# Kernel tuning notes

Hardware: AMD Instinct MI355X
Metric: run time of the kernel (lower is better)

## Reference

```python
import jax, jax.numpy as jnp
import numpy as np
from jax import lax

D = 512      # inter_dim
E = 768      # expand_dim
S = 256      # squeeze_dim
BUCKET = 64
N_BLOCK = 6

def layernorm(x, g, b, eps):
    m = jnp.mean(x, axis=-1, keepdims=True)
    v = jnp.mean(jnp.square(x - m), axis=-1, keepdims=True)
    return (x - m) / jnp.sqrt(v + eps) * g + b

def setup_inputs():
    key = jax.random.key(0)
    ks = jax.random.split(key, 12)
    B, N, IN = 4, 4096, 768
    def rn(k, shape, scale):
        return jax.random.normal(k, shape, dtype=jnp.float32) * scale
    return {
        "xs": jax.random.normal(ks[0], (B, N, IN), dtype=jnp.float32),
        # in1: Linear(IN, D) + LayerNorm(eps=1e-8) + LeakyReLU(0.1)
        "W_in": rn(ks[1], (IN, D), IN ** -0.5), "b_in": jnp.zeros(D),
        "ln_in_g": jnp.ones(D), "ln_in_b": jnp.zeros(D),
        # 6 GAU (FlashQuadAttention) blocks, params stacked on leading axis
        "blk_ln_g": jnp.ones((N_BLOCK, D)), "blk_ln_b": jnp.zeros((N_BLOCK, D)),
        "blk_Wuv": rn(ks[2], (N_BLOCK, D, 2 * E + S), D ** -0.5),
        "blk_buv": jnp.zeros((N_BLOCK, 2 * E + S)),
        "blk_gamma": jnp.ones((N_BLOCK, 2, S)) + rn(ks[3], (N_BLOCK, 2, S), 0.02),
        "blk_beta": rn(ks[4], (N_BLOCK, 2, S), 0.02),
        "blk_Wo": rn(ks[5], (N_BLOCK, E, D), E ** -0.5),
        "blk_bo": jnp.zeros((N_BLOCK, D)),
        # tr_layer (applied inside tree loop)
        "tr_W": rn(ks[6], (D, D), D ** -0.5), "tr_b": jnp.zeros(D),
        "tr_a": jnp.full((), 1e-6, dtype=jnp.float32),
        # out1 = TransLayer + Linear(D, out_dim)
        "tr2_W": rn(ks[7], (D, D), D ** -0.5), "tr2_b": jnp.zeros(D),
        "tr2_a": jnp.full((), 1e-6, dtype=jnp.float32),
        "out_W": rn(ks[8], (D, 2), D ** -0.5), "out_b": jnp.zeros(2),
    }

def reference(xs, W_in, b_in, ln_in_g, ln_in_b,
              blk_ln_g, blk_ln_b, blk_Wuv, blk_buv, blk_gamma, blk_beta,
              blk_Wo, blk_bo, tr_W, tr_b, tr_a, tr2_W, tr2_b, tr2_a,
              out_W, out_b):
    def subnet(h):  # h: [n_buckets, BUCKET, D]
        def step(h, p):
            lg, lb, Wuv, buv, gam, bet, Wo, bo = p
            n = layernorm(h, lg, lb, 1e-5)
            uvb = jax.nn.silu(n @ Wuv + buv)
            u, v, base = uvb[..., :E], uvb[..., E:2 * E], uvb[..., 2 * E:]
            q = base * gam[0] + bet[0]
            k = base * gam[1] + bet[1]
            Lq = h.shape[1]
            a = jnp.square(jax.nn.relu(jnp.einsum('gls,gms->glm', q, k) / Lq))
            o = jnp.einsum('glm,gme->gle', a, v) * u
            return h + o @ Wo + bo, None
        h, _ = lax.scan(step, h, (blk_ln_g, blk_ln_b, blk_Wuv, blk_buv,
                                  blk_gamma, blk_beta, blk_Wo, blk_bo))
        return h

    def tr_layer(x, W, b, a):
        return x + jax.nn.gelu(x @ W + b, approximate=False) * a

    def run_sample(x):  # x: [N, in_dim]
        h = layernorm(x @ W_in + b_in, ln_in_g, ln_in_b, 1e-8)
        h = jnp.where(h > 0, h, 0.1 * h)  # LeakyReLU(0.1)
        seq = h
        ys = []
        while seq.shape[0] > 1:  # static shapes -> unrolled tree levels
            ids = jnp.argsort(jnp.linalg.norm(seq, axis=-1))  # sort by L2 norm
            buckets = seq[ids].reshape(-1, BUCKET, D)
            gy = subnet(buckets).mean(axis=1)           # [n_buckets, D]
            ys.append(tr_layer(gy, tr_W, tr_b, tr_a).mean(axis=0))
            seq = gy
        return jnp.stack(ys, 0).mean(0)  # [D]

    y = jax.vmap(run_sample)(xs)          # [B, D]
    y = tr_layer(y, tr2_W, tr2_b, tr2_a)  # out1 TransLayer
    return y @ out_W + out_b              # [B, out_dim]
```

## Files before the change

kernel.cpp:

```cpp
#include <hip/hip_runtime.h>
#include <math.h>

#define R1C 16384

enum { OP_STORE = 0, OP_SILU = 1, OP_RESID = 2, OP_TR = 3 };

typedef _Float16 f16x8 __attribute__((ext_vector_type(8)));
typedef float f32x4 __attribute__((ext_vector_type(4)));

__device__ __forceinline__ float silu_f(float x) { return x / (1.0f + __expf(-x)); }
__device__ __forceinline__ float gelu_f(float x) {
  return 0.5f * x * (1.0f + erff(x * 0.70710678118654752f));
}

__device__ __forceinline__ void gll16(const void* g, const void* l) {
  __builtin_amdgcn_global_load_lds(
      (const __attribute__((address_space(1))) unsigned int*)g,
      (__attribute__((address_space(3))) unsigned int*)l, 16, 0, 0);
}

__device__ __forceinline__ void xcd_swizzle(int& bx, int& by) {
  int nx = gridDim.x;
  int nwg = nx * gridDim.y;
  int flat = by * nx + bx;
  int q = nwg >> 3, r = nwg & 7;
  int xcd = flat & 7, pos = flat >> 3;
  int lbid = (xcd < r) ? xcd * (q + 1) + pos
                       : r * (q + 1) + (xcd - r) * q + pos;
  bx = lbid % nx;
  by = lbid / nx;
}


__global__ __launch_bounds__(256) void gemm_f16(
    const _Float16* __restrict__ A, int lda,
    const _Float16* __restrict__ Bt, int ldb,
    float* __restrict__ C, int ldc, int K,
    const float* __restrict__ bias, int mode,
    const int* __restrict__ ids)
{
  const int BUF = 128 * 32;
  __shared__ _Float16 As[2 * BUF];
  __shared__ _Float16 Bs[2 * BUF];
  int bx = blockIdx.x, by = blockIdx.y;
  xcd_swizzle(bx, by);
  int tid = threadIdx.x;
  int lane = tid & 63, w = tid >> 6;
  int wm = w >> 1, wn = w & 1;
  int row0 = by * 128, col0 = bx * 128;

  int sm0 = tid >> 2;
  int sk  = (((tid & 3) - (sm0 >> 1)) & 3) * 8;
  const _Float16* gA[2];
  const _Float16* gB[2];
  gA[0] = A + (size_t)(row0 + sm0) * lda + sk;
  gA[1] = A + (size_t)(row0 + 64 + sm0) * lda + sk;
  gB[0] = Bt + (size_t)(col0 + sm0) * ldb + sk;
  gB[1] = Bt + (size_t)(col0 + 64 + sm0) * ldb + sk;
  const _Float16* lA[2] = { As + (size_t)(w * 64) * 8, As + (size_t)(256 + w * 64) * 8 };
  const _Float16* lB[2] = { Bs + (size_t)(w * 64) * 8, Bs + (size_t)(256 + w * 64) * 8 };

  int mrow = lane & 15, quad = lane >> 4;
  const f16x8* aptr[4];
  const f16x8* bptr[4];
#pragma unroll
  for (int t = 0; t < 4; ++t) {
    int ml = wm * 64 + t * 16 + mrow;
    aptr[t] = (const f16x8*)(As + (size_t)(ml * 4 + ((quad + (ml >> 1)) & 3)) * 8);
    int nl = wn * 64 + t * 16 + mrow;
    bptr[t] = (const f16x8*)(Bs + (size_t)(nl * 4 + ((quad + (nl >> 1)) & 3)) * 8);
  }

  f32x4 acc[4][4] = {};

  gll16(gA[0], lA[0]); gll16(gA[1], lA[1]);
  gll16(gB[0], lB[0]); gll16(gB[1], lB[1]);
  gA[0] += 32; gA[1] += 32; gB[0] += 32; gB[1] += 32;

  for (int kt = 0; kt < K; kt += 32) {
    int cur = (kt >> 5) & 1;
    __syncthreads();
    if (kt + 32 < K) {
      int nxo = (cur ^ 1) * BUF;
      gll16(gA[0], lA[0] + nxo); gll16(gA[1], lA[1] + nxo);
      gll16(gB[0], lB[0] + nxo); gll16(gB[1], lB[1] + nxo);
      gA[0] += 32; gA[1] += 32; gB[0] += 32; gB[1] += 32;
    }
    int fo = cur * (BUF / 8);
    f16x8 af[4], bfr[4];
#pragma unroll
    for (int t = 0; t < 4; ++t) { af[t] = *(aptr[t] + fo); bfr[t] = *(bptr[t] + fo); }
#pragma unroll
    for (int mt = 0; mt < 4; ++mt)
#pragma unroll
      for (int nt = 0; nt < 4; ++nt)
        acc[mt][nt] = __builtin_amdgcn_mfma_f32_16x16x32_f16(
            af[mt], bfr[nt], acc[mt][nt], 0, 0, 0);
  }

#pragma unroll
  for (int mt = 0; mt < 4; ++mt) {
#pragma unroll
    for (int nt = 0; nt < 4; ++nt) {
      int c = col0 + wn * 64 + nt * 16 + mrow;
      float bv = bias ? bias[c] : 0.0f;
#pragma unroll
      for (int reg = 0; reg < 4; ++reg) {
        int r = row0 + wm * 64 + mt * 16 + quad * 4 + reg;
        float val = acc[mt][nt][reg] + bv;
        if (mode == OP_STORE) {
          C[(size_t)r * ldc + c] = val;
        } else if (mode == OP_SILU) {
          C[(size_t)r * ldc + c] = silu_f(val);
        } else {
          int hr = ids ? ids[r] : r;
          C[(size_t)hr * ldc + c] += val;
        }
      }
    }
  }
}

__global__ __launch_bounds__(512) void gemm_f16_split(
    const _Float16* __restrict__ Ah, const _Float16* __restrict__ Al, int lda,
    const _Float16* __restrict__ Bh, const _Float16* __restrict__ Bl, int ldb,
    float* __restrict__ C, int ldc, int K, const float* __restrict__ bias)
{
  const int BUF = 128 * 32;
  __shared__ _Float16 AsH[2 * BUF], AsL[2 * BUF];
  __shared__ _Float16 BsH[2 * BUF], BsL[2 * BUF];
  int bx = blockIdx.x, by = blockIdx.y;
  xcd_swizzle(bx, by);
  int tid = threadIdx.x;
  int lane = tid & 63, w = tid >> 6;
  int wm = w >> 1, wn = w & 1;
  int row0 = by * 128, col0 = bx * 128;

  int m0 = tid >> 2;
  int k0e = (((tid & 3) - (m0 >> 1)) & 3) * 8;
  size_t a0 = (size_t)(row0 + m0) * lda + k0e;
  size_t b0 = (size_t)(col0 + m0) * ldb + k0e;
  size_t l0 = (size_t)(w * 64) * 8;

  int mrow = lane & 15, quad = lane >> 4;
  size_t aoff[2], boff[4];
#pragma unroll
  for (int t = 0; t < 2; ++t) {
    int ml = wm * 32 + t * 16 + mrow;
    aoff[t] = (size_t)(ml * 4 + ((quad + (ml >> 1)) & 3)) * 8;
  }
#pragma unroll
  for (int nt = 0; nt < 4; ++nt) {
    int nl = wn * 64 + nt * 16 + mrow;
    boff[nt] = (size_t)(nl * 4 + ((quad + (nl >> 1)) & 3)) * 8;
  }

  f32x4 acc[2][4] = {};

  gll16(Ah + a0, AsH + l0); gll16(Al + a0, AsL + l0);
  gll16(Bh + b0, BsH + l0); gll16(Bl + b0, BsL + l0);
  a0 += 32; b0 += 32;

  for (int kt = 0; kt < K; kt += 32) {
    int cur = (kt >> 5) & 1;
    __syncthreads();
    if (kt + 32 < K) {
      size_t o = (size_t)(cur ^ 1) * BUF;
      gll16(Ah + a0, AsH + l0 + o); gll16(Al + a0, AsL + l0 + o);
      gll16(Bh + b0, BsH + l0 + o); gll16(Bl + b0, BsL + l0 + o);
      a0 += 32; b0 += 32;
    }
    size_t o = (size_t)cur * BUF;
    f16x8 ah[2], al_[2], bh[4], bl[4];
#pragma unroll
    for (int t = 0; t < 2; ++t) {
      ah[t]  = *(const f16x8*)(AsH + aoff[t] + o);
      al_[t] = *(const f16x8*)(AsL + aoff[t] + o);
    }
#pragma unroll
    for (int nt = 0; nt < 4; ++nt) {
      bh[nt] = *(const f16x8*)(BsH + boff[nt] + o);
      bl[nt] = *(const f16x8*)(BsL + boff[nt] + o);
    }
#pragma unroll
    for (int mt = 0; mt < 2; ++mt)
#pragma unroll
      for (int nt = 0; nt < 4; ++nt) {
        acc[mt][nt] = __builtin_amdgcn_mfma_f32_16x16x32_f16(
            ah[mt], bh[nt], acc[mt][nt], 0, 0, 0);
        acc[mt][nt] = __builtin_amdgcn_mfma_f32_16x16x32_f16(
            ah[mt], bl[nt], acc[mt][nt], 0, 0, 0);
        acc[mt][nt] = __builtin_amdgcn_mfma_f32_16x16x32_f16(
            al_[mt], bh[nt], acc[mt][nt], 0, 0, 0);
      }
  }

#pragma unroll
  for (int mt = 0; mt < 2; ++mt)
#pragma unroll
    for (int nt = 0; nt < 4; ++nt) {
      int c = col0 + wn * 64 + nt * 16 + mrow;
      float bv = bias ? bias[c] : 0.0f;
#pragma unroll
      for (int reg = 0; reg < 4; ++reg) {
        int r = row0 + wm * 32 + mt * 16 + quad * 4 + reg;
        C[(size_t)r * ldc + c] = acc[mt][nt][reg] + bv;
      }
    }
}

__global__ __launch_bounds__(256) void gemm_f16_uvb(
    const _Float16* __restrict__ A, int lda,
    const _Float16* __restrict__ Bt,
    int c0, int nu,
    _Float16* __restrict__ ub, _Float16* __restrict__ vb, float* __restrict__ baseb,
    int CH, int K, const float* __restrict__ buv)
{
  const int BUF = 128 * 32;
  __shared__ _Float16 As[2 * BUF];
  __shared__ _Float16 Bs[2 * BUF];
  int bx = blockIdx.x, by = blockIdx.y;
  xcd_swizzle(bx, by);
  int tid = threadIdx.x;
  int lane = tid & 63, w = tid >> 6;
  int wm = w >> 1, wn = w & 1;
  int row0 = by * 128;

  int x = bx;
  int xl, regbase, ldc_, is_base = 0;
  _Float16* dst16 = nullptr;
  if (x < nu)            { xl = x;          regbase = c0;        dst16 = ub; ldc_ = CH; }
  else if (x < 2 * nu)   { xl = x - nu;     regbase = 768 + c0;  dst16 = vb; ldc_ = CH; }
  else                   { xl = x - 2 * nu; regbase = 1536;      is_base = 1; ldc_ = 256; }
  int brow0 = regbase + xl * 128;
  int dcol0 = xl * 128;

  int sm0 = tid >> 2;
  int sk  = (((tid & 3) - (sm0 >> 1)) & 3) * 8;
  const _Float16* gA[2];
  const _Float16* gB[2];
  gA[0] = A + (size_t)(row0 + sm0) * lda + sk;
  gA[1] = A + (size_t)(row0 + 64 + sm0) * lda + sk;
  gB[0] = Bt + (size_t)(brow0 + sm0) * 512 + sk;
  gB[1] = Bt + (size_t)(brow0 + 64 + sm0) * 512 + sk;
  const _Float16* lA[2] = { As + (size_t)(w * 64) * 8, As + (size_t)(256 + w * 64) * 8 };
  const _Float16* lB[2] = { Bs + (size_t)(w * 64) * 8, Bs + (size_t)(256 + w * 64) * 8 };

  int mrow = lane & 15, quad = lane >> 4;
  const f16x8* aptr[4];
  const f16x8* bptr[4];
#pragma unroll
  for (int t = 0; t < 4; ++t) {
    int ml = wm * 64 + t * 16 + mrow;
    aptr[t] = (const f16x8*)(As + (size_t)(ml * 4 + ((quad + (ml >> 1)) & 3)) * 8);
    int nl = wn * 64 + t * 16 + mrow;
    bptr[t] = (const f16x8*)(Bs + (size_t)(nl * 4 + ((quad + (nl >> 1)) & 3)) * 8);
  }

  f32x4 acc[4][4] = {};

  gll16(gA[0], lA[0]); gll16(gA[1], lA[1]);
  gll16(gB[0], lB[0]); gll16(gB[1], lB[1]);
  gA[0] += 32; gA[1] += 32; gB[0] += 32; gB[1] += 32;

  for (int kt = 0; kt < K; kt += 32) {
    int cur = (kt >> 5) & 1;
    __syncthreads();
    if (kt + 32 < K) {
      int nxo = (cur ^ 1) * BUF;
      gll16(gA[0], lA[0] + nxo); gll16(gA[1], lA[1] + nxo);
      gll16(gB[0], lB[0] + nxo); gll16(gB[1], lB[1] + nxo);
      gA[0] += 32; gA[1] += 32; gB[0] += 32; gB[1] += 32;
    }
    int fo = cur * (BUF / 8);
    f16x8 af[4], bfr[4];
#pragma unroll
    for (int t = 0; t < 4; ++t) { af[t] = *(aptr[t] + fo); bfr[t] = *(bptr[t] + fo); }
#pragma unroll
    for (int mt = 0; mt < 4; ++mt)
#pragma unroll
      for (int nt = 0; nt < 4; ++nt)
        acc[mt][nt] = __builtin_amdgcn_mfma_f32_16x16x32_f16(
            af[mt], bfr[nt], acc[mt][nt], 0, 0, 0);
  }

#pragma unroll
  for (int mt = 0; mt < 4; ++mt) {
#pragma unroll
    for (int nt = 0; nt < 4; ++nt) {
      int lc = wn * 64 + nt * 16 + mrow;
      float bv = buv[brow0 + lc];
#pragma unroll
      for (int reg = 0; reg < 4; ++reg) {
        int r = row0 + wm * 64 + mt * 16 + quad * 4 + reg;
        float val = silu_f(acc[mt][nt][reg] + bv);
        if (is_base) baseb[(size_t)r * 256 + dcol0 + lc] = val;
        else         dst16[(size_t)r * ldc_ + dcol0 + lc] = (_Float16)val;
      }
    }
  }
}

__global__ __launch_bounds__(256) void attnapply_fused(
    const float* __restrict__ base, const float* __restrict__ gb,
    const float* __restrict__ bb, const _Float16* __restrict__ v,
    const _Float16* __restrict__ u, _Float16* __restrict__ t, int CH, int ech)
{
  __shared__ _Float16 smem[3 * 64 * 72];
  _Float16* qs = smem;
  _Float16* ks = smem + 64 * 72;
  _Float16* al = smem + 2 * 64 * 72;
  _Float16* vT = smem;

  int bx = blockIdx.x, by = blockIdx.y;
  xcd_swizzle(bx, by);
  int g = by, tid = threadIdx.x;
  int e_lo = bx * ech, e_hi = e_lo + ech;
  int lane = tid & 63, w = tid >> 6;
  int mrow = lane & 15, quad = lane >> 4;
  int srow = tid >> 2, scol = (tid & 3) * 16;

  f32x4 acc[4] = {};
  for (int s0 = 0; s0 < 256; s0 += 64) {
    const float* bp = base + ((size_t)g * 64 + srow) * 256 + s0 + scol;
#pragma unroll
    for (int j4 = 0; j4 < 4; ++j4) {
      float4 xv = *(const float4*)(bp + j4 * 4);
      float xx[4] = {xv.x, xv.y, xv.z, xv.w};
#pragma unroll
      for (int j = 0; j < 4; ++j) {
        int s = s0 + scol + j4 * 4 + j;
        qs[srow * 72 + scol + j4 * 4 + j] = (_Float16)(xx[j] * gb[s] + bb[s]);
        ks[srow * 72 + scol + j4 * 4 + j] = (_Float16)(xx[j] * gb[256 + s] + bb[256 + s]);
      }
    }
    __syncthreads();
#pragma unroll
    for (int ks2 = 0; ks2 < 2; ++ks2) {
      f16x8 aq = *(const f16x8*)(qs + (w * 16 + mrow) * 72 + ks2 * 32 + quad * 8);
#pragma unroll
      for (int nt = 0; nt < 4; ++nt) {
        f16x8 bk = *(const f16x8*)(ks + (nt * 16 + mrow) * 72 + ks2 * 32 + quad * 8);
        acc[nt] = __builtin_amdgcn_mfma_f32_16x16x32_f16(aq, bk, acc[nt], 0, 0, 0);
      }
    }
    __syncthreads();
  }
#pragma unroll
  for (int nt = 0; nt < 4; ++nt)
#pragma unroll
    for (int reg = 0; reg < 4; ++reg) {
      float val = acc[nt][reg] * (1.0f / 64.0f);
      val = val > 0.0f ? val : 0.0f;
      val = val * val;
      al[(w * 16 + quad * 4 + reg) * 72 + nt * 16 + mrow] = (_Float16)val;
    }
  __syncthreads();

  for (int e0 = e_lo; e0 < e_hi; e0 += 64) {
    const _Float16* vp = v + ((size_t)g * 64 + srow) * CH + e0 + scol;
    f16x8 x0 = *(const f16x8*)vp;
    f16x8 x1 = *(const f16x8*)(vp + 8);
#pragma unroll
    for (int j = 0; j < 8; ++j) {
      vT[(scol + j) * 72 + srow] = x0[j];
      vT[(scol + 8 + j) * 72 + srow] = x1[j];
    }
    __syncthreads();
    f32x4 acc2[4] = {};
#pragma unroll
    for (int ks2 = 0; ks2 < 2; ++ks2) {
      f16x8 af = *(const f16x8*)(al + (w * 16 + mrow) * 72 + ks2 * 32 + quad * 8);
#pragma unroll
      for (int nt = 0; nt < 4; ++nt) {
        f16x8 bf = *(const f16x8*)(vT + (nt * 16 + mrow) * 72 + ks2 * 32 + quad * 8);
        acc2[nt] = __builtin_amdgcn_mfma_f32_16x16x32_f16(af, bf, acc2[nt], 0, 0, 0);
      }
    }
#pragma unroll
    for (int nt = 0; nt < 4; ++nt)
#pragma unroll
      for (int reg = 0; reg < 4; ++reg) {
        int row = w * 16 + quad * 4 + reg;
        int col = e0 + nt * 16 + mrow;
        size_t idx = ((size_t)g * 64 + row) * CH + col;
        t[idx] = (_Float16)(acc2[nt][reg] * (float)u[idx]);
      }
    __syncthreads();
  }
}

__global__ __launch_bounds__(256) void gemm_f32(
    const float* __restrict__ A, int lda,
    const float* __restrict__ B, int ldb,
    float* __restrict__ C, int ldc,
    int M, int N, int K,
    const float* __restrict__ bias, int mode,
    const int* __restrict__ ids,
    const float* __restrict__ X,
    const float* __restrict__ alpha)
{
  __shared__ float As[16][68];
  __shared__ float Bs[16][68];
  int tid = threadIdx.x;
  int tx = tid & 15, ty = tid >> 4;
  int col0 = blockIdx.x * 64, row0 = blockIdx.y * 64;
  float acc[4][4] = {};
  int arow = tid >> 2;
  int ak   = (tid & 3) * 4;
  int bk   = tid >> 4;
  int bn   = (tid & 15) * 4;

  for (int kt = 0; kt < K; kt += 16) {
    float4 av = make_float4(0.f, 0.f, 0.f, 0.f);
    if (row0 + arow < M)
      av = *(const float4*)&A[(size_t)(row0 + arow) * lda + kt + ak];
    As[ak + 0][arow] = av.x; As[ak + 1][arow] = av.y;
    As[ak + 2][arow] = av.z; As[ak + 3][arow] = av.w;
    float4 bv = *(const float4*)&B[(size_t)(kt + bk) * ldb + col0 + bn];
    *(float4*)&Bs[bk][bn] = bv;
    __syncthreads();
#pragma unroll
    for (int k = 0; k < 16; ++k) {
      const float4 a4 = *(const float4*)&As[k][ty * 4];
      const float4 b4 = *(const float4*)&Bs[k][tx * 4];
      float a_[4] = {a4.x, a4.y, a4.z, a4.w};
      float b_[4] = {b4.x, b4.y, b4.z, b4.w};
#pragma unroll
      for (int i = 0; i < 4; ++i)
#pragma unroll
        for (int j = 0; j < 4; ++j)
          acc[i][j] = fmaf(a_[i], b_[j], acc[i][j]);
    }
    __syncthreads();
  }

#pragma unroll
  for (int i = 0; i < 4; ++i) {
    int r = row0 + ty * 4 + i;
    if (r >= M) continue;
#pragma unroll
    for (int j = 0; j < 4; ++j) {
      int c = col0 + tx * 4 + j;
      float val = acc[i][j] + (bias ? bias[c] : 0.0f);
      if (mode == OP_STORE) {
        C[(size_t)r * ldc + c] = val;
      } else if (mode == OP_SILU) {
        C[(size_t)r * ldc + c] = silu_f(val);
      } else if (mode == OP_RESID) {
        int hr = ids ? ids[r] : r;
        C[(size_t)hr * ldc + c] += val;
      } else {
        C[(size_t)r * ldc + c] = X[(size_t)r * ldc + c] + gelu_f(val) * alpha[0];
      }
    }
  }
}

__global__ __launch_bounds__(256) void transpose_cast(
    const float* __restrict__ in, _Float16* __restrict__ out, int K, int N)
{
  in  += (size_t)blockIdx.z * K * N;
  out += (size_t)blockIdx.z * K * N;
  __shared__ float t[32][33];
  int k0 = blockIdx.y * 32, n0 = blockIdx.x * 32;
  int tx = threadIdx.x & 31, ty = threadIdx.x >> 5;
  for (int i = ty; i < 32; i += 8) {
    int k = k0 + i, n = n0 + tx;
    t[i][tx] = (k < K && n < N) ? in[(size_t)k * N + n] : 0.0f;
  }
  __syncthreads();
  for (int i = ty; i < 32; i += 8) {
    int n = n0 + i, k = k0 + tx;
    if (n < N && k < K) out[(size_t)n * K + k] = (_Float16)t[tx][i];
  }
}

__global__ __launch_bounds__(256) void transpose_split(
    const float* __restrict__ in, _Float16* __restrict__ hi,
    _Float16* __restrict__ lo, int K, int N)
{
  __shared__ float t[32][33];
  int k0 = blockIdx.y * 32, n0 = blockIdx.x * 32;
  int tx = threadIdx.x & 31, ty = threadIdx.x >> 5;
  for (int i = ty; i < 32; i += 8) {
    int k = k0 + i, n = n0 + tx;
    t[i][tx] = (k < K && n < N) ? in[(size_t)k * N + n] : 0.0f;
  }
  __syncthreads();
  for (int i = ty; i < 32; i += 8) {
    int n = n0 + i, k = k0 + tx;
    if (n < N && k < K) {
      float x = t[tx][i];
      _Float16 h = (_Float16)x;
      hi[(size_t)n * K + k] = h;
      lo[(size_t)n * K + k] = (_Float16)(x - (float)h);
    }
  }
}

__global__ __launch_bounds__(256) void split_f16_kernel(
    const float* __restrict__ in, _Float16* __restrict__ hi,
    _Float16* __restrict__ lo, int n)
{
  int i = blockIdx.x * 256 + threadIdx.x;
  if (i < n) {
    float x = in[i];
    _Float16 h = (_Float16)x;
    hi[i] = h;
    lo[i] = (_Float16)(x - (float)h);
  }
}

template <typename OUT>
__global__ __launch_bounds__(256) void ln_kernel(
    const float* __restrict__ src, const int* __restrict__ ids,
    OUT* __restrict__ dst, const float* __restrict__ g,
    const float* __restrict__ b, float eps, int leaky,
    float* __restrict__ nrm2)
{
  int r = blockIdx.x;
  int sr = ids ? ids[r] : r;
  int tid = threadIdx.x;
  float v0 = src[(size_t)sr * 512 + tid];
  float v1 = src[(size_t)sr * 512 + tid + 256];
  __shared__ float red[256], red2[256];
  red[tid] = v0 + v1;
  red2[tid] = v0 * v0 + v1 * v1;
  __syncthreads();
  for (int s = 128; s > 0; s >>= 1) {
    if (tid < s) { red[tid] += red[tid + s]; red2[tid] += red2[tid + s]; }
    __syncthreads();
  }
  float mean = red[0] * (1.0f / 512.0f);
  float var  = red2[0] * (1.0f / 512.0f) - mean * mean;
  float rs = rsqrtf(var + eps);
  float o0 = (v0 - mean) * rs * g[tid] + b[tid];
  float o1 = (v1 - mean) * rs * g[tid + 256] + b[tid + 256];
  if (leaky) {
    o0 = o0 > 0.0f ? o0 : 0.1f * o0;
    o1 = o1 > 0.0f ? o1 : 0.1f * o1;
  }
  dst[(size_t)r * 512 + tid] = (OUT)o0;
  dst[(size_t)r * 512 + tid + 256] = (OUT)o1;
  if (nrm2) {
    __syncthreads();
    red[tid] = o0 * o0 + o1 * o1;
    __syncthreads();
    for (int s = 128; s > 0; s >>= 1) {
      if (tid < s) red[tid] += red[tid + s];
      __syncthreads();
    }
    if (tid == 0) nrm2[r] = red[0];
  }
}

__global__ __launch_bounds__(128) void permute_rows(
    const float* __restrict__ src, const int* __restrict__ ids,
    float* __restrict__ dst)
{
  int r = blockIdx.x, sr = ids[r];
  const float4* s = (const float4*)(src + (size_t)sr * 512);
  float4* d = (float4*)(dst + (size_t)r * 512);
  d[threadIdx.x] = s[threadIdx.x];
}

__global__ __launch_bounds__(1024) void sort_kernel(const float* __restrict__ norm2,
                                                    int* __restrict__ ids)
{
  __shared__ float key[4096];
  __shared__ int   val[4096];
  int s = blockIdx.x, tid = threadIdx.x;
  for (int i = tid; i < 4096; i += 1024) { key[i] = norm2[s * 4096 + i]; val[i] = i; }
  __syncthreads();
  for (int len = 2; len <= 4096; len <<= 1) {
    for (int j = len >> 1; j > 0; j >>= 1) {
      for (int t = tid; t < 2048; t += 1024) {
        int i1 = (t << 1) - (t & (j - 1));
        int i2 = i1 + j;
        bool up = ((i1 & len) == 0);
        float ka = key[i1], kb = key[i2];
        int va = val[i1], vb = val[i2];
        bool gt = (ka > kb) || (ka == kb && va > vb);
        if (gt == up) {
          key[i1] = kb; key[i2] = ka;
          val[i1] = vb; val[i2] = va;
        }
      }
      __syncthreads();
    }
  }
  for (int i = tid; i < 4096; i += 1024) ids[s * 4096 + i] = s * 4096 + val[i];
}

__global__ __launch_bounds__(256) void bucketmean_kernel(
    const float* __restrict__ src, const int* __restrict__ ids,
    float* __restrict__ dst)
{
  int g = blockIdx.x, tid = threadIdx.x;
  float s0 = 0.0f, s1 = 0.0f;
  for (int i = 0; i < 64; ++i) {
    int r = g * 64 + i;
    if (ids) r = ids[r];
    s0 += src[(size_t)r * 512 + tid];
    s1 += src[(size_t)r * 512 + tid + 256];
  }
  dst[(size_t)g * 512 + tid] = s0 * (1.0f / 64.0f);
  dst[(size_t)g * 512 + tid + 256] = s1 * (1.0f / 64.0f);
}

__global__ void avg_kernel(const float* __restrict__ a, const float* __restrict__ b,
                           float* __restrict__ o, int n)
{
  int i = blockIdx.x * 256 + threadIdx.x;
  if (i < n) o[i] = 0.5f * (a[i] + b[i]);
}

__global__ void out_kernel(const float* __restrict__ y, const float* __restrict__ W,
                           const float* __restrict__ b, float* __restrict__ out)
{
  int tid = threadIdx.x;
  if (tid < 8) {
    int s = tid >> 1, j = tid & 1;
    float acc = b[j];
    for (int d = 0; d < 512; ++d) acc += y[s * 512 + d] * W[d * 2 + j];
    out[s * 2 + j] = acc;
  }
}

extern "C" void kernel_launch(void* const* d_in, const int* in_sizes, int n_in,
                              void* d_out, int out_size, void* d_ws, size_t ws_size,
                              hipStream_t stream)
{
  const float* xs       = (const float*)d_in[0];
  const float* W_in     = (const float*)d_in[1];
  const float* b_in     = (const float*)d_in[2];
  const float* ln_in_g  = (const float*)d_in[3];
  const float* ln_in_b  = (const float*)d_in[4];
  const float* blk_ln_g = (const float*)d_in[5];
  const float* blk_ln_b = (const float*)d_in[6];
  const float* blk_Wuv  = (const float*)d_in[7];
  const float* blk_buv  = (const float*)d_in[8];
  const float* blk_gam  = (const float*)d_in[9];
  const float* blk_bet  = (const float*)d_in[10];
  const float* blk_Wo   = (const float*)d_in[11];
  const float* blk_bo   = (const float*)d_in[12];
  const float* tr_W     = (const float*)d_in[13];
  const float* tr_b     = (const float*)d_in[14];
  const float* tr_a     = (const float*)d_in[15];
  const float* tr2_W    = (const float*)d_in[16];
  const float* tr2_b    = (const float*)d_in[17];
  const float* tr2_a    = (const float*)d_in[18];
  const float* out_W    = (const float*)d_in[19];
  const float* out_b    = (const float*)d_in[20];
  float* outp = (float*)d_out;

  const size_t R1 = R1C;

  char* wsb = (char*)d_ws;
  size_t off = 0;
  auto carve = [&](size_t bytes) {
    char* r = wsb + off;
    off = (off + bytes + 255) & ~(size_t)255;
    return (void*)r;
  };
  float* h      = (float*)carve(R1 * 512 * 4);
  float* hslot  = (float*)carve(R1 * 512 * 4);
  float* norm2b = (float*)carve(R1 * 4);
  int*   idsb   = (int*)carve(R1 * 4);
  float* gy     = (float*)carve((size_t)256 * 512 * 4);
  float* tl     = (float*)carve((size_t)256 * 512 * 4);
  float* gy2    = (float*)carve(4 * 512 * 4);
  float* ys0    = (float*)carve(4 * 512 * 4);
  float* ys1    = (float*)carve(4 * 512 * 4);
  float* yv     = (float*)carve(4 * 512 * 4);
  float* y2     = (float*)carve(4 * 512 * 4);
  _Float16* Wuvt = (_Float16*)carve((size_t)6 * 1792 * 512 * 2);
  _Float16* Wot  = (_Float16*)carve((size_t)6 * 512 * 768 * 2);
  size_t persistent = off;

  size_t stageA_sorted = 2 * R1 * 768 * 2 + 2 * (size_t)512 * 768 * 2 + R1 * 512 * 4 + 2048;
  size_t block768 = R1 * 256 * 4 + 3 * R1 * (size_t)768 * 2 + 2048;
  size_t un_sorted = stageA_sorted > block768 ? stageA_sorted : block768;
  bool sorted_mode = (persistent + un_sorted + 4096 <= ws_size);

  int CH = 768;
  bool splitA = true;
  if (!sorted_mode) {
    size_t stageA_fb = 2 * R1 * 768 * 2 + 2 * (size_t)512 * 768 * 2 + 1024;
    auto block_bytes = [&](size_t ch) {
      return R1 * 256 * 4 + 3 * R1 * ch * 2 + 2048;
    };
    CH = 0; splitA = false;
    const int cand[4] = {768, 384, 256, 128};
    for (int ci = 0; ci < 4; ++ci) {
      size_t bb2 = block_bytes(cand[ci]);
      size_t un2 = bb2 > stageA_fb ? bb2 : stageA_fb;
      if (persistent + un2 + 4096 <= ws_size) { CH = cand[ci]; splitA = true; break; }
    }
    if (!CH) {
      for (int ci = 0; ci < 4; ++ci)
        if (persistent + block_bytes(cand[ci]) + 4096 <= ws_size) { CH = cand[ci]; break; }
      if (!CH) CH = 128;
    }
  }
  int nu = CH / 128;
  int ech = CH >= 256 ? 256 : CH;
  int nch = CH / ech;

  char* un = wsb + ((persistent + 255) & ~(size_t)255);
  _Float16* xs_hi = (_Float16*)un;
  _Float16* xs_lo = xs_hi + R1 * 768;
  _Float16* Wt_hi = xs_lo + R1 * 768;
  _Float16* Wt_lo = Wt_hi + (size_t)512 * 768;
  float*    nbA   = sorted_mode ? (float*)(Wt_lo + (size_t)512 * 768) : hslot;
  float*    baseb = (float*)un;
  _Float16* ub    = (_Float16*)(un + R1 * 256 * 4);
  _Float16* vb    = ub + R1 * (size_t)CH;
  _Float16* tb    = vb + R1 * (size_t)CH;
  _Float16* nbuf  = sorted_mode ? tb : (_Float16*)hslot;
  float* hres = sorted_mode ? hslot : h;
  const int* blkids = sorted_mode ? nullptr : idsb;

  dim3 blk(256);
  dim3 blk5(512);

  transpose_cast<<<dim3(56, 16, 6), blk, 0, stream>>>(blk_Wuv, Wuvt, 512, 1792);
  transpose_cast<<<dim3(16, 24, 6), blk, 0, stream>>>(blk_Wo, Wot, 768, 512);

  if (splitA) {
    split_f16_kernel<<<(int)(R1 * 768 / 256), blk, 0, stream>>>(xs, xs_hi, xs_lo,
                                                                (int)(R1 * 768));
    transpose_split<<<dim3(16, 24, 1), blk, 0, stream>>>(W_in, Wt_hi, Wt_lo, 768, 512);
    gemm_f16_split<<<dim3(4, 128), blk5, 0, stream>>>(xs_hi, xs_lo, 768,
        Wt_hi, Wt_lo, 768, nbA, 512, 768, b_in);
  } else {
    gemm_f32<<<dim3(8, 256), blk, 0, stream>>>(xs, 768, W_in, 512, nbA, 512,
        16384, 512, 768, b_in, OP_STORE, nullptr, nullptr, nullptr);
  }
  ln_kernel<float><<<16384, 256, 0, stream>>>(nbA, nullptr, h, ln_in_g, ln_in_b,
                                              1e-8f, 1, norm2b);
  sort_kernel<<<4, 1024, 0, stream>>>(norm2b, idsb);
  if (sorted_mode)
    permute_rows<<<16384, 128, 0, stream>>>(h, idsb, hres);

  for (int b = 0; b < 6; ++b) {
    const _Float16* Wuv_t = Wuvt + (size_t)b * 1792 * 512;
    const float*    buv   = blk_buv + b * 1792;
    const _Float16* Wo_t  = Wot + (size_t)b * 512 * 768;
    ln_kernel<_Float16><<<16384, 256, 0, stream>>>(hres, blkids, nbuf,
        blk_ln_g + b * 512, blk_ln_b + b * 512, 1e-5f, 0, nullptr);
    for (int c0 = 0; c0 < 768; c0 += CH) {
      int incl = (c0 == 0) ? 2 : 0;
      gemm_f16_uvb<<<dim3(2 * nu + incl, 128), blk, 0, stream>>>(nbuf, 512, Wuv_t,
          c0, nu, ub, vb, baseb, CH, 512, buv);
      attnapply_fused<<<dim3(nch, 256), blk, 0, stream>>>(baseb, blk_gam + b * 512,
          blk_bet + b * 512, vb, ub, tb, CH, ech);
      const float* bo = (c0 + CH == 768) ? (blk_bo + b * 512) : nullptr;
      gemm_f16<<<dim3(4, 128), blk, 0, stream>>>(tb, CH, Wo_t + c0, 768,
          hres, 512, CH, bo, OP_RESID, blkids);
    }
  }
  bucketmean_kernel<<<256, 256, 0, stream>>>(hres, blkids, gy);

  gemm_f32<<<dim3(8, 4), blk, 0, stream>>>(gy, 512, tr_W, 512, tl, 512,
      256, 512, 512, tr_b, OP_TR, nullptr, gy, tr_a);
  bucketmean_kernel<<<4, 256, 0, stream>>>(tl, nullptr, ys0);

  for (int b = 0; b < 6; ++b) {
    const _Float16* Wuv_t = Wuvt + (size_t)b * 1792 * 512;
    const float*    buv   = blk_buv + b * 1792;
    const _Float16* Wo_t  = Wot + (size_t)b * 512 * 768;
    ln_kernel<_Float16><<<256, 256, 0, stream>>>(gy, nullptr, nbuf, blk_ln_g + b * 512,
                                                 blk_ln_b + b * 512, 1e-5f, 0, nullptr);
    for (int c0 = 0; c0 < 768; c0 += CH) {
      int incl = (c0 == 0) ? 2 : 0;
      gemm_f16_uvb<<<dim3(2 * nu + incl, 2), blk, 0, stream>>>(nbuf, 512, Wuv_t,
          c0, nu, ub, vb, baseb, CH, 512, buv);
      attnapply_fused<<<dim3(nch, 4), blk, 0, stream>>>(baseb, blk_gam + b * 512,
          blk_bet + b * 512, vb, ub, tb, CH, ech);
      const float* bo = (c0 + CH == 768) ? (blk_bo + b * 512) : nullptr;
      gemm_f16<<<dim3(4, 2), blk, 0, stream>>>(tb, CH, Wo_t + c0, 768,
          gy, 512, CH, bo, OP_RESID, nullptr);
    }
  }
  bucketmean_kernel<<<4, 256, 0, stream>>>(gy, nullptr, gy2);

  gemm_f32<<<dim3(8, 1), blk, 0, stream>>>(gy2, 512, tr_W, 512, ys1, 512,
      4, 512, 512, tr_b, OP_TR, nullptr, gy2, tr_a);
  avg_kernel<<<8, 256, 0, stream>>>(ys0, ys1, yv, 2048);
  gemm_f32<<<dim3(8, 1), blk, 0, stream>>>(yv, 512, tr2_W, 512, y2, 512,
      4, 512, 512, tr2_b, OP_TR, nullptr, yv, tr2_a);
  out_kernel<<<1, 64, 0, stream>>>(y2, out_W, out_b, outp);
}
```

Measured before the change: 1.747 ms.

## Triple-buffer LDS in f16 GEMM kernels with explicit vmcnt waits

Replaces the double-buffered global-to-LDS K loop in gemm_f16 and gemm_f16_uvb with a three-stage ring buffer that keeps two tiles in flight. It uses explicit s_waitcnt vmcnt(4) and a raw s_barrier instead of __syncthreads. Launch bounds now request 3 blocks per SIMD. The aim is to hide global load latency behind the MFMA work. In exchange, LDS use rises to 48KB per block, which may limit occupancy, and the hand-written waitcnt logic depends on the exact count of outstanding loads.

After: 1.757 ms. Within noise of the previous version (+0.5%).

```diff
diff --git a/kernel.cpp b/kernel.cpp
--- a/kernel.cpp
+++ b/kernel.cpp
@@ -32,7 +32,38 @@
 }
 
 
-__global__ __launch_bounds__(256) void gemm_f16(
+#define STAGE4(slot) do {                                            \
+    gll16(gAa, lAa + (slot) * BUF); gll16(gAb, lAb + (slot) * BUF);  \
+    gll16(gBa, lBa + (slot) * BUF); gll16(gBb, lBb + (slot) * BUF);  \
+    gAa += 32; gAb += 32; gBa += 32; gBb += 32; } while (0)
+
+#define KLOOP4()                                                          \
+  int ntile = K >> 5;                                                     \
+  STAGE4(0);                                                              \
+  if (ntile > 1) STAGE4(1);                                               \
+  int cur = 0;                                                            \
+  for (int t = 0; t < ntile; ++t) {                                       \
+    if (t + 1 < ntile) asm volatile("s_waitcnt vmcnt(4)" ::: "memory");   \
+    else               asm volatile("s_waitcnt vmcnt(0)" ::: "memory");   \
+    __builtin_amdgcn_s_barrier();                                         \
+    __builtin_amdgcn_sched_barrier(0);                                    \
+    if (t + 2 < ntile) { int pf = cur + 2; if (pf >= 3) pf -= 3; STAGE4(pf); } \
+    int fo = cur * (BUF / 8);                                             \
+    f16x8 af[4], bfr[4];                                                  \
+    _Pragma("unroll")                                                     \
+    for (int tt = 0; tt < 4; ++tt) af[tt] = *(aptr[tt] + fo);             \
+    _Pragma("unroll")                                                     \
+    for (int tt = 0; tt < 4; ++tt) bfr[tt] = *(bptr[tt] + fo);            \
+    _Pragma("unroll")                                                     \
+    for (int mt = 0; mt < 4; ++mt)                                        \
+      _Pragma("unroll")                                                   \
+      for (int nt = 0; nt < 4; ++nt)                                      \
+        acc[mt][nt] = __builtin_amdgcn_mfma_f32_16x16x32_f16(             \
+            af[mt], bfr[nt], acc[mt][nt], 0, 0, 0);                       \
+    cur = (cur == 2) ? 0 : cur + 1;                                       \
+  }
+
+__global__ __launch_bounds__(256, 3) void gemm_f16(
     const _Float16* __restrict__ A, int lda,
     const _Float16* __restrict__ Bt, int ldb,
     float* __restrict__ C, int ldc, int K,
@@ -40,8 +71,8 @@
     const int* __restrict__ ids)
 {
   const int BUF = 128 * 32;
-  __shared__ _Float16 As[2 * BUF];
-  __shared__ _Float16 Bs[2 * BUF];
+  __shared__ _Float16 As[3 * BUF];
+  __shared__ _Float16 Bs[3 * BUF];
   int bx = blockIdx.x, by = blockIdx.y;
   xcd_swizzle(bx, by);
   int tid = threadIdx.x;
@@ -49,16 +80,16 @@
   int wm = w >> 1, wn = w & 1;
   int row0 = by * 128, col0 = bx * 128;
 
-  int sm0 = tid >> 2;
-  int sk  = (((tid & 3) - (sm0 >> 1)) & 3) * 8;
-  const _Float16* gA[2];
-  const _Float16* gB[2];
-  gA[0] = A + (size_t)(row0 + sm0) * lda + sk;
-  gA[1] = A + (size_t)(row0 + 64 + sm0) * lda + sk;
-  gB[0] = Bt + (size_t)(col0 + sm0) * ldb + sk;
-  gB[1] = Bt + (size_t)(col0 + 64 + sm0) * ldb + sk;
-  const _Float16* lA[2] = { As + (size_t)(w * 64) * 8, As + (size_t)(256 + w * 64) * 8 };
-  const _Float16* lB[2] = { Bs + (size_t)(w * 64) * 8, Bs + (size_t)(256 + w * 64) * 8 };
+  int m0 = tid >> 2;
+  int k0e = (((tid & 3) - (m0 >> 1)) & 3) * 8;
+  const _Float16* gAa = A + (size_t)(row0 + m0) * lda + k0e;
+  const _Float16* gAb = A + (size_t)(row0 + 64 + m0) * lda + k0e;
+  const _Float16* gBa = Bt + (size_t)(col0 + m0) * ldb + k0e;
+  const _Float16* gBb = Bt + (size_t)(col0 + 64 + m0) * ldb + k0e;
+  const _Float16* lAa = As + (size_t)(w * 64) * 8;
+  const _Float16* lAb = As + (size_t)(256 + w * 64) * 8;
+  const _Float16* lBa = Bs + (size_t)(w * 64) * 8;
+  const _Float16* lBb = Bs + (size_t)(256 + w * 64) * 8;
 
   int mrow = lane & 15, quad = lane >> 4;
   const f16x8* aptr[4];
@@ -73,30 +104,7 @@
 
   f32x4 acc[4][4] = {};
 
-  gll16(gA[0], lA[0]); gll16(gA[1], lA[1]);
-  gll16(gB[0], lB[0]); gll16(gB[1], lB[1]);
-  gA[0] += 32; gA[1] += 32; gB[0] += 32; gB[1] += 32;
-
-  for (int kt = 0; kt < K; kt += 32) {
-    int cur = (kt >> 5) & 1;
-    __syncthreads();
-    if (kt + 32 < K) {
-      int nxo = (cur ^ 1) * BUF;
-      gll16(gA[0], lA[0] + nxo); gll16(gA[1], lA[1] + nxo);
-      gll16(gB[0], lB[0] + nxo); gll16(gB[1], lB[1] + nxo);
-      gA[0] += 32; gA[1] += 32; gB[0] += 32; gB[1] += 32;
-    }
-    int fo = cur * (BUF / 8);
-    f16x8 af[4], bfr[4];
-#pragma unroll
-    for (int t = 0; t < 4; ++t) { af[t] = *(aptr[t] + fo); bfr[t] = *(bptr[t] + fo); }
-#pragma unroll
-    for (int mt = 0; mt < 4; ++mt)
-#pragma unroll
-      for (int nt = 0; nt < 4; ++nt)
-        acc[mt][nt] = __builtin_amdgcn_mfma_f32_16x16x32_f16(
-            af[mt], bfr[nt], acc[mt][nt], 0, 0, 0);
-  }
+  KLOOP4();
 
 #pragma unroll
   for (int mt = 0; mt < 4; ++mt) {
@@ -209,7 +217,7 @@
     }
 }
 
-__global__ __launch_bounds__(256) void gemm_f16_uvb(
+__global__ __launch_bounds__(256, 3) void gemm_f16_uvb(
     const _Float16* __restrict__ A, int lda,
     const _Float16* __restrict__ Bt,
     int c0, int nu,
@@ -217,8 +225,8 @@
     int CH, int K, const float* __restrict__ buv)
 {
   const int BUF = 128 * 32;
-  __shared__ _Float16 As[2 * BUF];
-  __shared__ _Float16 Bs[2 * BUF];
+  __shared__ _Float16 As[3 * BUF];
+  __shared__ _Float16 Bs[3 * BUF];
   int bx = blockIdx.x, by = blockIdx.y;
   xcd_swizzle(bx, by);
   int tid = threadIdx.x;
@@ -235,16 +243,16 @@
   int brow0 = regbase + xl * 128;
   int dcol0 = xl * 128;
 
-  int sm0 = tid >> 2;
-  int sk  = (((tid & 3) - (sm0 >> 1)) & 3) * 8;
-  const _Float16* gA[2];
-  const _Float16* gB[2];
-  gA[0] = A + (size_t)(row0 + sm0) * lda + sk;
-  gA[1] = A + (size_t)(row0 + 64 + sm0) * lda + sk;
-  gB[0] = Bt + (size_t)(brow0 + sm0) * 512 + sk;
-  gB[1] = Bt + (size_t)(brow0 + 64 + sm0) * 512 + sk;
-  const _Float16* lA[2] = { As + (size_t)(w * 64) * 8, As + (size_t)(256 + w * 64) * 8 };
-  const _Float16* lB[2] = { Bs + (size_t)(w * 64) * 8, Bs + (size_t)(256 + w * 64) * 8 };
+  int m0 = tid >> 2;
+  int k0e = (((tid & 3) - (m0 >> 1)) & 3) * 8;
+  const _Float16* gAa = A + (size_t)(row0 + m0) * lda + k0e;
+  const _Float16* gAb = A + (size_t)(row0 + 64 + m0) * lda + k0e;
+  const _Float16* gBa = Bt + (size_t)(brow0 + m0) * 512 + k0e;
+  const _Float16* gBb = Bt + (size_t)(brow0 + 64 + m0) * 512 + k0e;
+  const _Float16* lAa = As + (size_t)(w * 64) * 8;
+  const _Float16* lAb = As + (size_t)(256 + w * 64) * 8;
+  const _Float16* lBa = Bs + (size_t)(w * 64) * 8;
+  const _Float16* lBb = Bs + (size_t)(256 + w * 64) * 8;
 
   int mrow = lane & 15, quad = lane >> 4;
   const f16x8* aptr[4];
@@ -259,30 +267,7 @@
 
   f32x4 acc[4][4] = {};
 
-  gll16(gA[0], lA[0]); gll16(gA[1], lA[1]);
-  gll16(gB[0], lB[0]); gll16(gB[1], lB[1]);
-  gA[0] += 32; gA[1] += 32; gB[0] += 32; gB[1] += 32;
-
-  for (int kt = 0; kt < K; kt += 32) {
-    int cur = (kt >> 5) & 1;
-    __syncthreads();
-    if (kt + 32 < K) {
-      int nxo = (cur ^ 1) * BUF;
-      gll16(gA[0], lA[0] + nxo); gll16(gA[1], lA[1] + nxo);
-      gll16(gB[0], lB[0] + nxo); gll16(gB[1], lB[1] + nxo);
-      gA[0] += 32; gA[1] += 32; gB[0] += 32; gB[1] += 32;
-    }
-    int fo = cur * (BUF / 8);
-    f16x8 af[4], bfr[4];
-#pragma unroll
-    for (int t = 0; t < 4; ++t) { af[t] = *(aptr[t] + fo); bfr[t] = *(bptr[t] + fo); }
-#pragma unroll
-    for (int mt = 0; mt < 4; ++mt)
-#pragma unroll
-      for (int nt = 0; nt < 4; ++nt)
-        acc[mt][nt] = __builtin_amdgcn_mfma_f32_16x16x32_f16(
-            af[mt], bfr[nt], acc[mt][nt], 0, 0, 0);
-  }
+  KLOOP4();
 
 #pragma unroll
   for (int mt = 0; mt < 4; ++mt) {
```
